# Optimization experiments

Hardware: AMD Instinct MI355X
Metric: run time of the kernel (lower is better)

Reference implementation:

```python
import jax, jax.numpy as jnp
import numpy as np

N_NODES = 50000
N_EDGES = 800000
D_FEAT = 64
K_HOPS = 8


def setup_inputs() -> dict:
    key = jax.random.key(0)
    k1, k2 = jax.random.split(key)
    feature = jax.random.normal(k1, (N_NODES, D_FEAT), dtype=jnp.float32)
    edge_index = jax.random.randint(k2, (2, N_EDGES), 0, N_NODES, dtype=jnp.int32)
    return {"feature": feature, "edge_index": edge_index}


def reference(feature, edge_index):
    # with A_hat = D^{-1/2} (A + I) D^{-1/2} (add_remaining_self_loops + sym_norm).
    n = feature.shape[0]
    src, dst = edge_index[0], edge_index[1]
    # add_remaining_self_loops: drop any existing self-loop edges (weight -> 0)
    # and append a self loop of weight fill_value=1 for every node. Zeroing the
    # weight is mathematically identical to removing the edge.
    ew = jnp.where(src == dst, 0.0, 1.0).astype(feature.dtype)
    loop = jnp.arange(n, dtype=src.dtype)
    row = jnp.concatenate([src, loop])          # message source (x_j)
    col = jnp.concatenate([dst, loop])          # aggregation target (i)
    w = jnp.concatenate([ew, jnp.ones((n,), dtype=feature.dtype)])
    # symmetric normalization: deg over row, norm = d^-1/2[row] * w * d^-1/2[col]
    deg = jax.ops.segment_sum(w, row, num_segments=n)
    deg_inv_sqrt = jnp.where(deg > 0, jax.lax.rsqrt(deg), 0.0)
    norm = deg_inv_sqrt[row] * w * deg_inv_sqrt[col]  # [E+N]

    xs = [feature]
    x = feature
    for _ in range(K_HOPS):  # small fixed K, structural loop
        # gather-scale-scatter_add: out[i] = sum_{(j,i) in E} norm * x[j]
        x = jax.ops.segment_sum(norm[:, None] * x[row], col, num_segments=n)
        xs.append(x)
    return jnp.concatenate(xs, axis=1)  # [N, (K+1)*D]
```

## Files before the change

### kernel.cpp

```cpp
#include <hip/hip_runtime.h>
#include <hip/hip_fp16.h>

#define N_NODES 50000
#define N_EDGES 800000
#define D_FEAT 64
#define K_HOPS 8
#define OUT_STRIDE ((K_HOPS + 1) * D_FEAT)
#define NPART 128
#define CHUNK (N_EDGES / NPART)
#define NWORD (N_NODES / 2)

#define SCAN_WORDS 512
#define SCAN_NB ((NWORD + SCAN_WORDS - 1) / SCAN_WORDS)

#define ALIGN256(x) (((x) + 255) & ~(size_t)255)
static const size_t OFF_P     = 0;
static const size_t OFF_BASES = OFF_P + (size_t)NPART * NWORD * 4;
static const size_t OFF_OFF   = ALIGN256(OFF_BASES + (size_t)NPART * N_NODES * 4);
static const size_t OFF_BSUM  = ALIGN256(OFF_OFF   + (size_t)(N_NODES + 1) * 4);
static const size_t OFF_TOTW  = ALIGN256(OFF_BSUM  + 64 * 4);
static const size_t OFF_DINV  = ALIGN256(OFF_TOTW  + (size_t)NWORD * 4);
static const size_t OFF_CSR   = ALIGN256(OFF_DINV  + (size_t)N_NODES * 4);
static const size_t OFF_XA    = ALIGN256(OFF_CSR   + (size_t)N_EDGES * 4);
static const size_t OFF_XB    = ALIGN256(OFF_XA + (size_t)(N_NODES + 1) * D_FEAT * 2);

__device__ __forceinline__ unsigned pack_h2(float a, float b) {
    union { __half2 h; unsigned u; } c;
    c.h = __floats2half2_rn(a, b);
    return c.u;
}
__device__ __forceinline__ float2 unpack_h2(unsigned u) {
    union { unsigned u; __half2 h; } c;
    c.u = u;
    return __half22float2(c.h);
}


__global__ __launch_bounds__(256, 1) void k_hist(const int* __restrict__ src,
                                                 const int* __restrict__ dst,
                                                 unsigned* __restrict__ p) {
    __shared__ unsigned h[NWORD];
    int t = threadIdx.x;
    int base = blockIdx.x * CHUNK;
    for (int w = t; w < NWORD; w += 256) h[w] = 0u;
    __syncthreads();
    for (int j = t; j < CHUNK; j += 256) {
        int s = src[base + j], d = dst[base + j];
        if (s != d) {
            atomicAdd(&h[s >> 1], 1u << (8 * (s & 1)));
            atomicAdd(&h[d >> 1], 65536u << (8 * (d & 1)));
        }
    }
    __syncthreads();
    unsigned* o = p + (size_t)blockIdx.x * NWORD;
    for (int w = t; w < NWORD; w += 256) o[w] = h[w];
}

__global__ void k_sum(const unsigned* __restrict__ p, float* __restrict__ dinv,
                      unsigned* __restrict__ totW) {
    int w = blockIdx.x * blockDim.x + threadIdx.x;
    if (w >= NWORD) return;
    unsigned s0 = 0, s1 = 0, s2 = 0, s3 = 0;
    #pragma unroll 4
    for (int c = 0; c < NPART; c += 4) {
        s0 += p[(size_t)(c + 0) * NWORD + w];
        s1 += p[(size_t)(c + 1) * NWORD + w];
        s2 += p[(size_t)(c + 2) * NWORD + w];
        s3 += p[(size_t)(c + 3) * NWORD + w];
    }
    unsigned s = (s0 + s1) + (s2 + s3);
    dinv[2 * w + 0] = rsqrtf((float)((s & 0xffu) + 1u));
    dinv[2 * w + 1] = rsqrtf((float)(((s >> 8) & 0xffu) + 1u));
    totW[w] = ((s >> 16) & 0xffu) | ((s >> 24) << 16);
}

__global__ void k_scan_sums(const unsigned* __restrict__ totW, int* __restrict__ bsum) {
    __shared__ int lds[256];
    int b = blockIdx.x, t = threadIdx.x;
    int wend = min((b + 1) * SCAN_WORDS, NWORD);
    int tot = 0;
    for (int w = b * SCAN_WORDS + t; w < wend; w += 256) {
        unsigned v = totW[w];
        tot += (int)(v & 0xffffu) + (int)(v >> 16);
    }
    lds[t] = tot; __syncthreads();
    for (int str = 128; str > 0; str >>= 1) {
        if (t < str) lds[t] += lds[t + str];
        __syncthreads();
    }
    if (t == 0) bsum[b] = lds[0];
}

__global__ void k_scan_top(int* __restrict__ bsum) {
    int lane = threadIdx.x;
    int orig = (lane < SCAN_NB) ? bsum[lane] : 0;
    int v = orig;
    for (int d = 1; d < 64; d <<= 1) {
        int u = __shfl_up(v, d, 64);
        if (lane >= d) v += u;
    }
    if (lane < SCAN_NB) bsum[lane] = v - orig;
}

__global__ void k_scan_downA(const unsigned* __restrict__ totW, const int* __restrict__ bsum,
                             int* __restrict__ off) {
    __shared__ int lds[256];
    int b = blockIdx.x, t = threadIdx.x;
    int w0 = b * SCAN_WORDS + 2 * t;
    unsigned t0 = (w0 < NWORD) ? totW[w0] : 0u;
    unsigned t1 = (w0 + 1 < NWORD) ? totW[w0 + 1] : 0u;
    int n[4] = { (int)(t0 & 0xffffu), (int)(t0 >> 16),
                 (int)(t1 & 0xffffu), (int)(t1 >> 16) };
    int tsum = (n[0] + n[1]) + (n[2] + n[3]);
    lds[t] = tsum; __syncthreads();
    int x = tsum;
    for (int d = 1; d < 256; d <<= 1) {
        int u = (t >= d) ? lds[t - d] : 0;
        __syncthreads();
        x += u;
        lds[t] = x;
        __syncthreads();
    }
    int pfx = (x - tsum) + bsum[b];
    #pragma unroll
    for (int j = 0; j < 4; ++j) {
        int node = 2 * w0 + j;
        if (node < N_NODES) {
            off[node] = pfx;
            pfx += n[j];
        } else if (node == N_NODES) {
            off[node] = pfx;
        }
    }
}

__global__ void k_bases(const unsigned* __restrict__ p, const int* __restrict__ off,
                        int* __restrict__ bases) {
    int node = blockIdx.x * blockDim.x + threadIdx.x;
    if (node >= N_NODES) return;
    int w = node >> 1;
    int sh = 16 + 8 * (node & 1);
    int acc = off[node];
    for (int c = 0; c < NPART; ++c) {
        bases[(size_t)c * N_NODES + node] = acc;
        acc += (int)((p[(size_t)c * NWORD + w] >> sh) & 0xffu);
    }
}

__global__ __launch_bounds__(256, 1) void k_scatter(const int* __restrict__ src,
                                                    const int* __restrict__ dst,
                                                    const int* __restrict__ bases,
                                                    int* __restrict__ csr) {
    __shared__ unsigned h[NWORD];
    int t = threadIdx.x;
    int base = blockIdx.x * CHUNK;
    const int* bp = bases + (size_t)blockIdx.x * N_NODES;
    for (int w = t; w < NWORD; w += 256) h[w] = 0u;
    __syncthreads();
    for (int j = t; j < CHUNK; j += 256) {
        int s = src[base + j], d = dst[base + j];
        if (s == d) continue;
        unsigned old = atomicAdd(&h[d >> 1], (d & 1) ? 65536u : 1u);
        unsigned pw = (d & 1) ? (old >> 16) : (old & 0xffffu);
        csr[bp[d] + (int)pw] = s;
    }
}


__global__ void k_x0(const float4* __restrict__ feat4, float4* __restrict__ out4,
                     uint2* __restrict__ y0, const float* __restrict__ dinv) {
    int t = blockIdx.x * blockDim.x + threadIdx.x;
    if (t >= (N_NODES + 1) * 16) return;
    int row = t >> 4;
    if (row < N_NODES) {
        float4 v = feat4[t];
        out4[(size_t)row * (OUT_STRIDE / 4) + (t & 15)] = v;
        float di = dinv[row];
        uint2 w;
        w.x = pack_h2(v.x * di, v.y * di);
        w.y = pack_h2(v.z * di, v.w * di);
        y0[t] = w;
    } else {
        y0[t] = make_uint2(0u, 0u);
    }
}

template <bool WRITE_HALF>
__global__ __launch_bounds__(256) void k_hop4(
    const uint2* __restrict__ yin,
    float4* __restrict__ outcol4,
    uint2* __restrict__ yout,
    const int* __restrict__ off, const int* __restrict__ csr,
    const float* __restrict__ dinv) {
    int qw = (blockIdx.x * blockDim.x + threadIdx.x) >> 6;
    int lane = threadIdx.x & 63;
    int f = lane & 15;
    int node = qw * 4 + (lane >> 4);
    int e0 = off[node], e1 = off[node + 1];
    float di = dinv[node];
    uint2 sv = yin[node * 16 + f];
    float2 lo = unpack_h2(sv.x), hi = unpack_h2(sv.y);
    float a0 = lo.x, a1 = lo.y, a2 = hi.x, a3 = hi.y;

    int nm = e1 - e0;
    #pragma unroll
    for (int d = 32; d; d >>= 1) nm = max(nm, __shfl_xor(nm, d, 64));

    auto FETCH = [&](int j) -> int {
        int idx = e0 + j;
        int c = csr[idx < e1 ? idx : 0];
        return (idx < e1) ? c : N_NODES;
    };

    int c0 = FETCH(0), c1 = FETCH(1), c2 = FETCH(2), c3 = FETCH(3);
    for (int j = 0; j < nm; j += 4) {
        int d0 = FETCH(j + 4), d1 = FETCH(j + 5), d2 = FETCH(j + 6), d3 = FETCH(j + 7);
        uint2 q0 = yin[c0 * 16 + f];
        uint2 q1 = yin[c1 * 16 + f];
        uint2 q2 = yin[c2 * 16 + f];
        uint2 q3 = yin[c3 * 16 + f];
        float2 t;
        t = unpack_h2(q0.x); a0 += t.x; a1 += t.y;
        t = unpack_h2(q0.y); a2 += t.x; a3 += t.y;
        t = unpack_h2(q1.x); a0 += t.x; a1 += t.y;
        t = unpack_h2(q1.y); a2 += t.x; a3 += t.y;
        t = unpack_h2(q2.x); a0 += t.x; a1 += t.y;
        t = unpack_h2(q2.y); a2 += t.x; a3 += t.y;
        t = unpack_h2(q3.x); a0 += t.x; a1 += t.y;
        t = unpack_h2(q3.y); a2 += t.x; a3 += t.y;
        c0 = d0; c1 = d1; c2 = d2; c3 = d3;
    }

    outcol4[(size_t)node * (OUT_STRIDE / 4) + f] =
        make_float4(di * a0, di * a1, di * a2, di * a3);
    if (WRITE_HALF) {
        float di2 = di * di;
        uint2 w;
        w.x = pack_h2(di2 * a0, di2 * a1);
        w.y = pack_h2(di2 * a2, di2 * a3);
        yout[node * 16 + f] = w;
        if (blockIdx.x == 0 && threadIdx.x < 16)
            yout[N_NODES * 16 + threadIdx.x] = make_uint2(0u, 0u);
    }
}


extern "C" void kernel_launch(void* const* d_in, const int* in_sizes, int n_in,
                              void* d_out, int out_size, void* d_ws, size_t ws_size,
                              hipStream_t stream) {
    const float* feature = (const float*)d_in[0];
    const int* edge = (const int*)d_in[1];
    const int* src = edge;
    const int* dst = edge + N_EDGES;
    float* out = (float*)d_out;
    char* ws = (char*)d_ws;

    unsigned* p     = (unsigned*)(ws + OFF_P);
    int*      bases = (int*)(ws + OFF_BASES);
    int*      off   = (int*)(ws + OFF_OFF);
    int*      bsum  = (int*)(ws + OFF_BSUM);
    unsigned* totW  = (unsigned*)(ws + OFF_TOTW);
    float*    dinv  = (float*)(ws + OFF_DINV);
    int*      csr   = (int*)(ws + OFF_CSR);
    uint2*    xa    = (uint2*)(ws + OFF_XA);
    uint2*    xb    = (uint2*)(ws + OFF_XB);

    const int TB = 256;
    const int NB_NODES = (N_NODES + TB - 1) / TB;
    k_hist<<<NPART, 256, 0, stream>>>(src, dst, p);
    k_sum<<<(NWORD + TB - 1) / TB, TB, 0, stream>>>(p, dinv, totW);
    k_x0<<<((N_NODES + 1) * 16 + TB - 1) / TB, TB, 0, stream>>>(
        (const float4*)feature, (float4*)out, xb, dinv);
    k_scan_sums<<<SCAN_NB, 256, 0, stream>>>(totW, bsum);
    k_scan_top<<<1, 64, 0, stream>>>(bsum);
    k_scan_downA<<<SCAN_NB, 256, 0, stream>>>(totW, bsum, off);
    k_bases<<<NB_NODES, TB, 0, stream>>>(p, off, bases);
    k_scatter<<<NPART, 256, 0, stream>>>(src, dst, bases, csr);
    const int hop_blocks = (N_NODES / 4) * 64 / TB;
    for (int k = 1; k <= K_HOPS; ++k) {
        const uint2* yin = (k & 1) ? xb : xa;
        uint2* yout      = (k & 1) ? xa : xb;
        float4* outcol4 = (float4*)out + (size_t)k * 16;
        if (k < K_HOPS)
            k_hop4<true><<<hop_blocks, TB, 0, stream>>>(yin, outcol4, yout, off, csr, dinv);
        else
            k_hop4<false><<<hop_blocks, TB, 0, stream>>>(yin, outcol4, nullptr, off, csr, dinv);
    }
}
```

Before: 326.8 us.

## Split half-precision features into two 32-column planes, one hop pass per plane

Stores the fp16 propagated features as two separate planes of 32 columns each, and runs each hop as two kernel launches, one per plane. Each wavefront now handles 8 nodes with 8 lanes per node, so each gathered row is 64 bytes instead of 128. The aim is a smaller working set per launch (about 3.2MB per plane), so gathers hit in L2 more often. The cost is that CSR offsets and indices are read twice per hop, and the launch count doubles.

```diff
diff --git a/kernel.cpp b/kernel.cpp
--- a/kernel.cpp
+++ b/kernel.cpp
@@ -12,6 +12,9 @@
 
 #define SCAN_WORDS 512
 #define SCAN_NB ((NWORD + SCAN_WORDS - 1) / SCAN_WORDS)
+
+#define NOCT (N_NODES / 8)
+#define HALF_U2 ((size_t)(N_NODES + 1) * 8)
 
 #define ALIGN256(x) (((x) + 255) & ~(size_t)255)
 static const size_t OFF_P     = 0;
@@ -22,7 +25,7 @@
 static const size_t OFF_DINV  = ALIGN256(OFF_TOTW  + (size_t)NWORD * 4);
 static const size_t OFF_CSR   = ALIGN256(OFF_DINV  + (size_t)N_NODES * 4);
 static const size_t OFF_XA    = ALIGN256(OFF_CSR   + (size_t)N_EDGES * 4);
-static const size_t OFF_XB    = ALIGN256(OFF_XA + (size_t)(N_NODES + 1) * D_FEAT * 2);
+static const size_t OFF_XB    = ALIGN256(OFF_XA + (size_t)2 * HALF_U2 * 8);
 
 __device__ __forceinline__ unsigned pack_h2(float a, float b) {
     union { __half2 h; unsigned u; } c;
@@ -171,34 +174,36 @@
                      uint2* __restrict__ y0, const float* __restrict__ dinv) {
     int t = blockIdx.x * blockDim.x + threadIdx.x;
     if (t >= (N_NODES + 1) * 16) return;
-    int row = t >> 4;
+    int row = t >> 4, c = t & 15;
+    uint2* slot = y0 + (size_t)(c >> 3) * HALF_U2 + (size_t)row * 8 + (c & 7);
     if (row < N_NODES) {
         float4 v = feat4[t];
-        out4[(size_t)row * (OUT_STRIDE / 4) + (t & 15)] = v;
+        out4[(size_t)row * (OUT_STRIDE / 4) + c] = v;
         float di = dinv[row];
         uint2 w;
         w.x = pack_h2(v.x * di, v.y * di);
         w.y = pack_h2(v.z * di, v.w * di);
-        y0[t] = w;
+        *slot = w;
     } else {
-        y0[t] = make_uint2(0u, 0u);
+        *slot = make_uint2(0u, 0u);
     }
 }
 
 template <bool WRITE_HALF>
-__global__ __launch_bounds__(256) void k_hop4(
+__global__ __launch_bounds__(256) void k_hop8(
     const uint2* __restrict__ yin,
     float4* __restrict__ outcol4,
     uint2* __restrict__ yout,
     const int* __restrict__ off, const int* __restrict__ csr,
     const float* __restrict__ dinv) {
-    int qw = (blockIdx.x * blockDim.x + threadIdx.x) >> 6;
+    int ow = (blockIdx.x * blockDim.x + threadIdx.x) >> 6;
+    if (ow >= NOCT) return;
     int lane = threadIdx.x & 63;
-    int f = lane & 15;
-    int node = qw * 4 + (lane >> 4);
+    int f = lane & 7;
+    int node = ow * 8 + (lane >> 3);
     int e0 = off[node], e1 = off[node + 1];
     float di = dinv[node];
-    uint2 sv = yin[node * 16 + f];
+    uint2 sv = yin[(size_t)node * 8 + f];
     float2 lo = unpack_h2(sv.x), hi = unpack_h2(sv.y);
     float a0 = lo.x, a1 = lo.y, a2 = hi.x, a3 = hi.y;
 
@@ -215,10 +220,10 @@
     int c0 = FETCH(0), c1 = FETCH(1), c2 = FETCH(2), c3 = FETCH(3);
     for (int j = 0; j < nm; j += 4) {
         int d0 = FETCH(j + 4), d1 = FETCH(j + 5), d2 = FETCH(j + 6), d3 = FETCH(j + 7);
-        uint2 q0 = yin[c0 * 16 + f];
-        uint2 q1 = yin[c1 * 16 + f];
-        uint2 q2 = yin[c2 * 16 + f];
-        uint2 q3 = yin[c3 * 16 + f];
+        uint2 q0 = yin[(size_t)c0 * 8 + f];
+        uint2 q1 = yin[(size_t)c1 * 8 + f];
+        uint2 q2 = yin[(size_t)c2 * 8 + f];
+        uint2 q3 = yin[(size_t)c3 * 8 + f];
         float2 t;
         t = unpack_h2(q0.x); a0 += t.x; a1 += t.y;
         t = unpack_h2(q0.y); a2 += t.x; a3 += t.y;
@@ -238,9 +243,9 @@
         uint2 w;
         w.x = pack_h2(di2 * a0, di2 * a1);
         w.y = pack_h2(di2 * a2, di2 * a3);
-        yout[node * 16 + f] = w;
-        if (blockIdx.x == 0 && threadIdx.x < 16)
-            yout[N_NODES * 16 + threadIdx.x] = make_uint2(0u, 0u);
+        yout[(size_t)node * 8 + f] = w;
+        if (blockIdx.x == 0 && threadIdx.x < 8)
+            yout[(size_t)N_NODES * 8 + threadIdx.x] = make_uint2(0u, 0u);
     }
 }
 
@@ -276,14 +281,18 @@
     k_scan_downA<<<SCAN_NB, 256, 0, stream>>>(totW, bsum, off);
     k_bases<<<NB_NODES, TB, 0, stream>>>(p, off, bases);
     k_scatter<<<NPART, 256, 0, stream>>>(src, dst, bases, csr);
-    const int hop_blocks = (N_NODES / 4) * 64 / TB;
+    const int hop_blocks = (NOCT * 64 + TB - 1) / TB;
     for (int k = 1; k <= K_HOPS; ++k) {
-        const uint2* yin = (k & 1) ? xb : xa;
-        uint2* yout      = (k & 1) ? xa : xb;
-        float4* outcol4 = (float4*)out + (size_t)k * 16;
-        if (k < K_HOPS)
-            k_hop4<true><<<hop_blocks, TB, 0, stream>>>(yin, outcol4, yout, off, csr, dinv);
-        else
-            k_hop4<false><<<hop_blocks, TB, 0, stream>>>(yin, outcol4, nullptr, off, csr, dinv);
-    }
-}
+        uint2* yinb  = (k & 1) ? xb : xa;
+        uint2* youtb = (k & 1) ? xa : xb;
+        for (int h = 0; h < 2; ++h) {
+            const uint2* yin = yinb + (size_t)h * HALF_U2;
+            uint2* yout      = youtb + (size_t)h * HALF_U2;
+            float4* outcol4 = (float4*)out + (size_t)k * 16 + h * 8;
+            if (k < K_HOPS)
+                k_hop8<true><<<hop_blocks, TB, 0, stream>>>(yin, outcol4, yout, off, csr, dinv);
+            else
+                k_hop8<false><<<hop_blocks, TB, 0, stream>>>(yin, outcol4, nullptr, off, csr, dinv);
+        }
+    }
+}
```

Measured after the change: 383.0 us. +17.2%, slower.

## Use 8 lanes per node with 16-byte gathers and shuffled neighbor indices

Applied to the files above, without the earlier changes.

The hop kernel now maps 8 lanes to each node, so each lane loads 16 bytes (8 halfs) per neighbor row and a wavefront covers 8 nodes instead of 4. Neighbor indices are loaded cooperatively, one per lane, and broadcast with shuffles, replacing the redundant per-lane CSR loads. The inner loop is unrolled by 8 neighbors for more memory parallelism. The trade-offs are higher register pressure from eight accumulators and eight outstanding uint4 loads, and more divergence waste because 8 nodes share a wavefront-wide max degree.

```diff
diff --git a/kernel.cpp b/kernel.cpp
--- a/kernel.cpp
+++ b/kernel.cpp
@@ -12,6 +12,8 @@
 
 #define SCAN_WORDS 512
 #define SCAN_NB ((NWORD + SCAN_WORDS - 1) / SCAN_WORDS)
+
+#define NOCT (N_NODES / 8)
 
 #define ALIGN256(x) (((x) + 255) & ~(size_t)255)
 static const size_t OFF_P     = 0;
@@ -186,61 +188,101 @@
 }
 
 template <bool WRITE_HALF>
-__global__ __launch_bounds__(256) void k_hop4(
-    const uint2* __restrict__ yin,
+__global__ __launch_bounds__(256) void k_hopv(
+    const uint4* __restrict__ yin,
     float4* __restrict__ outcol4,
-    uint2* __restrict__ yout,
+    uint4* __restrict__ yout,
     const int* __restrict__ off, const int* __restrict__ csr,
     const float* __restrict__ dinv) {
-    int qw = (blockIdx.x * blockDim.x + threadIdx.x) >> 6;
+    int ow = (blockIdx.x * blockDim.x + threadIdx.x) >> 6;
+    if (ow >= NOCT) return;
     int lane = threadIdx.x & 63;
-    int f = lane & 15;
-    int node = qw * 4 + (lane >> 4);
+    int f = lane & 7;
+    int node = ow * 8 + (lane >> 3);
     int e0 = off[node], e1 = off[node + 1];
+    int deg = e1 - e0;
     float di = dinv[node];
-    uint2 sv = yin[node * 16 + f];
-    float2 lo = unpack_h2(sv.x), hi = unpack_h2(sv.y);
-    float a0 = lo.x, a1 = lo.y, a2 = hi.x, a3 = hi.y;
-
-    int nm = e1 - e0;
+    uint4 sv = yin[(size_t)node * 8 + f];
+    float2 u;
+    float a0, a1, a2, a3, a4, a5, a6, a7;
+    u = unpack_h2(sv.x); a0 = u.x; a1 = u.y;
+    u = unpack_h2(sv.y); a2 = u.x; a3 = u.y;
+    u = unpack_h2(sv.z); a4 = u.x; a5 = u.y;
+    u = unpack_h2(sv.w); a6 = u.x; a7 = u.y;
+
+    int nm = deg;
     #pragma unroll
     for (int d = 32; d; d >>= 1) nm = max(nm, __shfl_xor(nm, d, 64));
 
-    auto FETCH = [&](int j) -> int {
-        int idx = e0 + j;
-        int c = csr[idx < e1 ? idx : 0];
-        return (idx < e1) ? c : N_NODES;
-    };
-
-    int c0 = FETCH(0), c1 = FETCH(1), c2 = FETCH(2), c3 = FETCH(3);
-    for (int j = 0; j < nm; j += 4) {
-        int d0 = FETCH(j + 4), d1 = FETCH(j + 5), d2 = FETCH(j + 6), d3 = FETCH(j + 7);
-        uint2 q0 = yin[c0 * 16 + f];
-        uint2 q1 = yin[c1 * 16 + f];
-        uint2 q2 = yin[c2 * 16 + f];
-        uint2 q3 = yin[c3 * 16 + f];
-        float2 t;
-        t = unpack_h2(q0.x); a0 += t.x; a1 += t.y;
-        t = unpack_h2(q0.y); a2 += t.x; a3 += t.y;
-        t = unpack_h2(q1.x); a0 += t.x; a1 += t.y;
-        t = unpack_h2(q1.y); a2 += t.x; a3 += t.y;
-        t = unpack_h2(q2.x); a0 += t.x; a1 += t.y;
-        t = unpack_h2(q2.y); a2 += t.x; a3 += t.y;
-        t = unpack_h2(q3.x); a0 += t.x; a1 += t.y;
-        t = unpack_h2(q3.y); a2 += t.x; a3 += t.y;
-        c0 = d0; c1 = d1; c2 = d2; c3 = d3;
-    }
-
-    outcol4[(size_t)node * (OUT_STRIDE / 4) + f] =
-        make_float4(di * a0, di * a1, di * a2, di * a3);
+    int gbase = lane & ~7;
+
+    int cvec = csr[min(e0 + f, N_EDGES - 1)];
+    for (int j = 0; j < nm; j += 8) {
+        int cnext = csr[min(e0 + j + 8 + f, N_EDGES - 1)];
+        int v0 = (j + 0 < deg) ? __shfl(cvec, gbase + 0, 64) : N_NODES;
+        int v1 = (j + 1 < deg) ? __shfl(cvec, gbase + 1, 64) : N_NODES;
+        int v2 = (j + 2 < deg) ? __shfl(cvec, gbase + 2, 64) : N_NODES;
+        int v3 = (j + 3 < deg) ? __shfl(cvec, gbase + 3, 64) : N_NODES;
+        int v4 = (j + 4 < deg) ? __shfl(cvec, gbase + 4, 64) : N_NODES;
+        int v5 = (j + 5 < deg) ? __shfl(cvec, gbase + 5, 64) : N_NODES;
+        int v6 = (j + 6 < deg) ? __shfl(cvec, gbase + 6, 64) : N_NODES;
+        int v7 = (j + 7 < deg) ? __shfl(cvec, gbase + 7, 64) : N_NODES;
+        uint4 q0 = yin[(size_t)v0 * 8 + f];
+        uint4 q1 = yin[(size_t)v1 * 8 + f];
+        uint4 q2 = yin[(size_t)v2 * 8 + f];
+        uint4 q3 = yin[(size_t)v3 * 8 + f];
+        uint4 q4 = yin[(size_t)v4 * 8 + f];
+        uint4 q5 = yin[(size_t)v5 * 8 + f];
+        uint4 q6 = yin[(size_t)v6 * 8 + f];
+        uint4 q7 = yin[(size_t)v7 * 8 + f];
+        u = unpack_h2(q0.x); a0 += u.x; a1 += u.y;
+        u = unpack_h2(q0.y); a2 += u.x; a3 += u.y;
+        u = unpack_h2(q0.z); a4 += u.x; a5 += u.y;
+        u = unpack_h2(q0.w); a6 += u.x; a7 += u.y;
+        u = unpack_h2(q1.x); a0 += u.x; a1 += u.y;
+        u = unpack_h2(q1.y); a2 += u.x; a3 += u.y;
+        u = unpack_h2(q1.z); a4 += u.x; a5 += u.y;
+        u = unpack_h2(q1.w); a6 += u.x; a7 += u.y;
+        u = unpack_h2(q2.x); a0 += u.x; a1 += u.y;
+        u = unpack_h2(q2.y); a2 += u.x; a3 += u.y;
+        u = unpack_h2(q2.z); a4 += u.x; a5 += u.y;
+        u = unpack_h2(q2.w); a6 += u.x; a7 += u.y;
+        u = unpack_h2(q3.x); a0 += u.x; a1 += u.y;
+        u = unpack_h2(q3.y); a2 += u.x; a3 += u.y;
+        u = unpack_h2(q3.z); a4 += u.x; a5 += u.y;
+        u = unpack_h2(q3.w); a6 += u.x; a7 += u.y;
+        u = unpack_h2(q4.x); a0 += u.x; a1 += u.y;
+        u = unpack_h2(q4.y); a2 += u.x; a3 += u.y;
+        u = unpack_h2(q4.z); a4 += u.x; a5 += u.y;
+        u = unpack_h2(q4.w); a6 += u.x; a7 += u.y;
+        u = unpack_h2(q5.x); a0 += u.x; a1 += u.y;
+        u = unpack_h2(q5.y); a2 += u.x; a3 += u.y;
+        u = unpack_h2(q5.z); a4 += u.x; a5 += u.y;
+        u = unpack_h2(q5.w); a6 += u.x; a7 += u.y;
+        u = unpack_h2(q6.x); a0 += u.x; a1 += u.y;
+        u = unpack_h2(q6.y); a2 += u.x; a3 += u.y;
+        u = unpack_h2(q6.z); a4 += u.x; a5 += u.y;
+        u = unpack_h2(q6.w); a6 += u.x; a7 += u.y;
+        u = unpack_h2(q7.x); a0 += u.x; a1 += u.y;
+        u = unpack_h2(q7.y); a2 += u.x; a3 += u.y;
+        u = unpack_h2(q7.z); a4 += u.x; a5 += u.y;
+        u = unpack_h2(q7.w); a6 += u.x; a7 += u.y;
+        cvec = cnext;
+    }
+
+    size_t orow = (size_t)node * (OUT_STRIDE / 4) + 2 * f;
+    outcol4[orow]     = make_float4(di * a0, di * a1, di * a2, di * a3);
+    outcol4[orow + 1] = make_float4(di * a4, di * a5, di * a6, di * a7);
     if (WRITE_HALF) {
         float di2 = di * di;
-        uint2 w;
+        uint4 w;
         w.x = pack_h2(di2 * a0, di2 * a1);
         w.y = pack_h2(di2 * a2, di2 * a3);
-        yout[node * 16 + f] = w;
-        if (blockIdx.x == 0 && threadIdx.x < 16)
-            yout[N_NODES * 16 + threadIdx.x] = make_uint2(0u, 0u);
+        w.z = pack_h2(di2 * a4, di2 * a5);
+        w.w = pack_h2(di2 * a6, di2 * a7);
+        yout[(size_t)node * 8 + f] = w;
+        if (blockIdx.x == 0 && threadIdx.x < 8)
+            yout[(size_t)N_NODES * 8 + threadIdx.x] = make_uint4(0u, 0u, 0u, 0u);
     }
 }
 
@@ -262,28 +304,28 @@
     unsigned* totW  = (unsigned*)(ws + OFF_TOTW);
     float*    dinv  = (float*)(ws + OFF_DINV);
     int*      csr   = (int*)(ws + OFF_CSR);
-    uint2*    xa    = (uint2*)(ws + OFF_XA);
-    uint2*    xb    = (uint2*)(ws + OFF_XB);
+    uint4*    xa    = (uint4*)(ws + OFF_XA);
+    uint4*    xb    = (uint4*)(ws + OFF_XB);
 
     const int TB = 256;
     const int NB_NODES = (N_NODES + TB - 1) / TB;
     k_hist<<<NPART, 256, 0, stream>>>(src, dst, p);
     k_sum<<<(NWORD + TB - 1) / TB, TB, 0, stream>>>(p, dinv, totW);
     k_x0<<<((N_NODES + 1) * 16 + TB - 1) / TB, TB, 0, stream>>>(
-        (const float4*)feature, (float4*)out, xb, dinv);
+        (const float4*)feature, (float4*)out, (uint2*)xb, dinv);
     k_scan_sums<<<SCAN_NB, 256, 0, stream>>>(totW, bsum);
     k_scan_top<<<1, 64, 0, stream>>>(bsum);
     k_scan_downA<<<SCAN_NB, 256, 0, stream>>>(totW, bsum, off);
     k_bases<<<NB_NODES, TB, 0, stream>>>(p, off, bases);
     k_scatter<<<NPART, 256, 0, stream>>>(src, dst, bases, csr);
-    const int hop_blocks = (N_NODES / 4) * 64 / TB;
+    const int hop_blocks = (NOCT * 64 + TB - 1) / TB;
     for (int k = 1; k <= K_HOPS; ++k) {
-        const uint2* yin = (k & 1) ? xb : xa;
-        uint2* yout      = (k & 1) ? xa : xb;
+        const uint4* yin = (k & 1) ? xb : xa;
+        uint4* yout      = (k & 1) ? xa : xb;
         float4* outcol4 = (float4*)out + (size_t)k * 16;
         if (k < K_HOPS)
-            k_hop4<true><<<hop_blocks, TB, 0, stream>>>(yin, outcol4, yout, off, csr, dinv);
+            k_hopv<true><<<hop_blocks, TB, 0, stream>>>(yin, outcol4, yout, off, csr, dinv);
         else
-            k_hop4<false><<<hop_blocks, TB, 0, stream>>>(yin, outcol4, nullptr, off, csr, dinv);
-    }
-}
+            k_hopv<false><<<hop_blocks, TB, 0, stream>>>(yin, outcol4, nullptr, off, csr, dinv);
+    }
+}
```

Measured after the change: 318.8 us. 2.5% less time.
